# Performance work log

Hardware: AMD Instinct MI355X
Metric: run time of the kernel (lower is better)

Reference implementation:

```python
import jax, jax.numpy as jnp
import numpy as np

EPS = 1e-5
NUM_HEADS = 16

def layernorm(x, g, b):
    mu = jnp.mean(x, axis=-1, keepdims=True)
    var = jnp.mean(jnp.square(x - mu), axis=-1, keepdims=True)
    return (x - mu) * jax.lax.rsqrt(var + EPS) * g + b

def setup_inputs() -> dict:
    key = jax.random.key(0)
    ks = jax.random.split(key, 5)
    B, N, C = 2, 2048, 1024
    s_in = 1.0 / np.sqrt(C)
    return {
        "x": jax.random.normal(ks[0], (B, N, C), jnp.float32),
        "ln1_g": jnp.ones((C,), jnp.float32),
        "ln1_b": jnp.zeros((C,), jnp.float32),
        "w_qk": jax.random.normal(ks[1], (C, 2 * C), jnp.float32) * s_in,
        "w_v": jax.random.normal(ks[2], (C, C), jnp.float32) * s_in,
        "ln2_g": jnp.ones((C,), jnp.float32),
        "ln2_b": jnp.zeros((C,), jnp.float32),
        "w_proj": jax.random.normal(ks[3], (C, C), jnp.float32) * s_in,
        "b_proj": jnp.zeros((C,), jnp.float32),
    }

def reference(x, ln1_g, ln1_b, w_qk, w_v, ln2_g, ln2_b, w_proj, b_proj):
    B, N, C = x.shape
    H = NUM_HEADS
    hd = C // H
    scale = hd ** (-0.5)
    xn = layernorm(x, ln1_g, ln1_b)
    # qk: [B,N,2C] -> q,k each [B,H,N,hd]
    qk = (xn @ w_qk).reshape(B, N, 2, H, hd).transpose(2, 0, 3, 1, 4)
    q, k = qk[0], qk[1]
    v = (xn @ w_v).reshape(B, N, H, hd).transpose(0, 2, 1, 3)  # [B,H,N,hd]
    attn = jnp.einsum("bhqd,bhkd->bhqk", q, k) * scale
    attn = jax.nn.softmax(attn, axis=-1)
    out = jnp.einsum("bhqk,bhkd->bhqd", attn, v)  # [B,H,N,hd]
    out = out.transpose(0, 2, 1, 3).reshape(B, N, C)
    out = layernorm(out, ln2_g, ln2_b)
    return out @ w_proj + b_proj
```

## Files before the change

kernel.cpp:

```cpp
#include <hip/hip_runtime.h>
#include <hip/hip_bf16.h>


typedef __attribute__((ext_vector_type(8))) short short8;
typedef __attribute__((ext_vector_type(4))) short short4v;
typedef __attribute__((ext_vector_type(4))) float float4v;
typedef __attribute__((ext_vector_type(4))) unsigned uint4v;

__device__ __forceinline__ unsigned short f2bf(float f) {
    unsigned u = __builtin_bit_cast(unsigned, f);
    return (unsigned short)((u + 0x7FFFu + ((u >> 16) & 1u)) >> 16);
}
__device__ __forceinline__ unsigned packbf2(float lo, float hi) {
    return __builtin_amdgcn_perm(__builtin_bit_cast(unsigned, hi) + 0x8000u,
                                 __builtin_bit_cast(unsigned, lo) + 0x8000u,
                                 0x07060302u);
}
__device__ __forceinline__ void gll16(const unsigned short* g, unsigned short* l) {
    __builtin_amdgcn_global_load_lds(
        (const __attribute__((address_space(1))) unsigned int*)g,
        (__attribute__((address_space(3))) unsigned int*)l, 16, 0, 0);
}

__global__ __launch_bounds__(256) void prep(
    const float* __restrict__ x, const float* __restrict__ g1, const float* __restrict__ b1,
    const float* __restrict__ w_qk, const float* __restrict__ w_v,
    const float* __restrict__ w_proj, const float* __restrict__ g2,
    const float* __restrict__ b2,
    unsigned short* __restrict__ xn, unsigned short* __restrict__ wqkvT,
    unsigned short* __restrict__ wgT, float* __restrict__ u, float* __restrict__ w0) {
    __shared__ float sh[32 * 33];
    const int bid = blockIdx.x, tid = threadIdx.x;
    if (bid < 4096) {
        const float4 v = reinterpret_cast<const float4*>(x + (size_t)bid * 1024)[tid];
        float s  = v.x + v.y + v.z + v.w;
        float sq = v.x * v.x + v.y * v.y + v.z * v.z + v.w * v.w;
#pragma unroll
        for (int off = 32; off >= 1; off >>= 1) {
            s  += __shfl_xor(s, off, 64);
            sq += __shfl_xor(sq, off, 64);
        }
        const int w = tid >> 6, lane = tid & 63;
        if (lane == 0) { sh[w] = s; sh[4 + w] = sq; }
        __syncthreads();
        s  = sh[0] + sh[1] + sh[2] + sh[3];
        sq = sh[4] + sh[5] + sh[6] + sh[7];
        const float mu = s * (1.f / 1024.f);
        const float rstd = rsqrtf(sq * (1.f / 1024.f) - mu * mu + 1e-5f);
        const float4 gv = reinterpret_cast<const float4*>(g1)[tid];
        const float4 bv = reinterpret_cast<const float4*>(b1)[tid];
        ushort4 o;
        o.x = f2bf((v.x - mu) * rstd * gv.x + bv.x);
        o.y = f2bf((v.y - mu) * rstd * gv.y + bv.y);
        o.z = f2bf((v.z - mu) * rstd * gv.z + bv.z);
        o.w = f2bf((v.w - mu) * rstd * gv.w + bv.w);
        *reinterpret_cast<ushort4*>(&xn[(size_t)bid * 1024 + tid * 4]) = o;
    } else {
        const float* in; unsigned short* out; int Cc, bx, by; bool doU = false;
        if (bid < 6144)      { int t = bid - 4096; in = w_qk;   out = wqkvT;               Cc = 2048; bx = t & 63; by = t >> 6; }
        else if (bid < 7168) { int t = bid - 6144; in = w_v;    out = wqkvT + 2048 * 1024; Cc = 1024; bx = t & 31; by = t >> 5; }
        else                 { int t = bid - 7168; in = w_proj; out = wgT; doU = true;     Cc = 1024; bx = t & 31; by = t >> 5; }
        const int c0 = bx * 32, r0 = by * 32;
        const int tx = tid & 31, ty = tid >> 5;
#pragma unroll
        for (int i = 0; i < 32; i += 8)
            sh[(ty + i) * 33 + tx] = in[(size_t)(r0 + ty + i) * Cc + c0 + tx];
        __syncthreads();
        const float scale = doU ? g2[r0 + tx] : 1.f;
        const float b2v   = doU ? b2[r0 + tx] : 0.f;
#pragma unroll
        for (int i = 0; i < 32; i += 8) {
            const float raw = sh[tx * 33 + ty + i];
            const float sc  = raw * scale;
            out[(size_t)(c0 + ty + i) * 1024 + r0 + tx] = f2bf(sc);
            if (doU) {
                float pu = sc, pw = raw * b2v;
#pragma unroll
                for (int off = 1; off <= 16; off <<= 1) {
                    pu += __shfl_xor(pu, off, 64);
                    pw += __shfl_xor(pw, off, 64);
                }
                if (tx == 0) {
                    atomicAdd(&u[c0 + ty + i], pu);
                    atomicAdd(&w0[c0 + ty + i], pw);
                }
            }
        }
    }
}

__global__ __launch_bounds__(512) void gemm_qkv(const unsigned short* __restrict__ A,
                                                const unsigned short* __restrict__ Bt,
                                                unsigned short* __restrict__ qb,
                                                unsigned short* __restrict__ kb,
                                                unsigned short* __restrict__ vT) {
    __shared__ unsigned short As[2 * 256 * 64];
    __shared__ unsigned short Bs[2 * 192 * 64];
    const int tid = threadIdx.x, lane = tid & 63, w = tid >> 6;
    const int wm = (w >> 1) * 64, wn = (w & 1) * 96;
    const int quad = lane >> 4, l16 = lane & 15;
    const int ls = lane >> 3, sg = lane & 7;
    const int m0 = blockIdx.y * 256, n0 = blockIdx.x * 192;

    float4v acc[4][6];
#pragma unroll
    for (int mi = 0; mi < 4; mi++)
#pragma unroll
        for (int ni = 0; ni < 6; ni++) acc[mi][ni] = float4v{0.f, 0.f, 0.f, 0.f};

    const int g = (sg ^ ls) * 8;
#pragma unroll
    for (int i = 0; i < 4; i++)
        gll16(&A[(size_t)(m0 + w * 32 + i * 8 + ls) * 1024 + g], &As[(w * 32 + i * 8) * 64]);
#pragma unroll
    for (int i = 0; i < 3; i++)
        gll16(&Bt[(size_t)(n0 + w * 24 + i * 8 + ls) * 1024 + g], &Bs[(w * 24 + i * 8) * 64]);

#pragma unroll 1
    for (int s = 0; s < 16; s++) {
        __syncthreads();
        if (s + 1 < 16) {
            const int k0 = (s + 1) << 6;
            unsigned short* Ad = As + (((s + 1) & 1) << 14);
            unsigned short* Bd = Bs + (((s + 1) & 1) * 12288);
#pragma unroll
            for (int i = 0; i < 4; i++)
                gll16(&A[(size_t)(m0 + w * 32 + i * 8 + ls) * 1024 + k0 + g],
                      &Ad[(w * 32 + i * 8) * 64]);
#pragma unroll
            for (int i = 0; i < 3; i++)
                gll16(&Bt[(size_t)(n0 + w * 24 + i * 8 + ls) * 1024 + k0 + g],
                      &Bd[(w * 24 + i * 8) * 64]);
        }
        const unsigned short* Ac = As + ((s & 1) << 14);
        const unsigned short* Bc = Bs + ((s & 1) * 12288);
#pragma unroll
        for (int ks = 0; ks < 2; ks++) {
            short8 af[4], bfr[6];
#pragma unroll
            for (int mi = 0; mi < 4; mi++) {
                const int r = wm + mi * 16 + l16;
                af[mi] = *reinterpret_cast<const short8*>(
                    &Ac[r * 64 + ((ks * 4 + quad) ^ (r & 7)) * 8]);
            }
#pragma unroll
            for (int ni = 0; ni < 6; ni++) {
                const int r = wn + ni * 16 + l16;
                bfr[ni] = *reinterpret_cast<const short8*>(
                    &Bc[r * 64 + ((ks * 4 + quad) ^ (r & 7)) * 8]);
            }
#pragma unroll
            for (int mi = 0; mi < 4; mi++)
#pragma unroll
                for (int ni = 0; ni < 6; ni++)
                    acc[mi][ni] = __builtin_amdgcn_mfma_f32_16x16x32_bf16(
                        af[mi], bfr[ni], acc[mi][ni], 0, 0, 0);
        }
    }

    const float QSCALE = 0.125f * 1.4426950408889634f;
#pragma unroll
    for (int mi = 0; mi < 4; mi++) {
        const int row0 = m0 + wm + mi * 16 + quad * 4;
        const int b = row0 >> 11, nq = row0 & 2047;
#pragma unroll
        for (int ni = 0; ni < 6; ni++) {
            const int col = n0 + wn + ni * 16 + l16;
            if (col < 1024) {
                const int h = col >> 6, d = col & 63;
#pragma unroll
                for (int r = 0; r < 4; r++)
                    qb[(((size_t)b * 16 + h) * 2048 + nq + r) * 64 + d] =
                        f2bf(acc[mi][ni][r] * QSCALE);
            } else if (col < 2048) {
                const int c = col - 1024, h = c >> 6, d = c & 63;
#pragma unroll
                for (int r = 0; r < 4; r++)
                    kb[(((size_t)b * 16 + h) * 2048 + nq + r) * 64 + d] = f2bf(acc[mi][ni][r]);
            } else {
                const int c = col - 2048, h = c >> 6, d = c & 63;
                const short4v sv = {(short)f2bf(acc[mi][ni][0]), (short)f2bf(acc[mi][ni][1]),
                                    (short)f2bf(acc[mi][ni][2]), (short)f2bf(acc[mi][ni][3])};
                *reinterpret_cast<short4v*>(
                    &vT[(((size_t)b * 16 + h) * 64 + d) * 2048 + nq]) = sv;
            }
        }
    }
}

__global__ __launch_bounds__(256) void flash_attn(const unsigned short* __restrict__ qbuf,
                                                  const unsigned short* __restrict__ kb,
                                                  const unsigned short* __restrict__ vT,
                                                  unsigned short* __restrict__ attn,
                                                  float2* __restrict__ part) {
    __shared__ unsigned short Ks[2][64 * 64];
    __shared__ unsigned short Vs[2][64 * 64];
    const int tid = threadIdx.x, lane = tid & 63, w = tid >> 6;
    const int quad = lane >> 4, l16 = lane & 15;
    const int ls = lane >> 3, sg = lane & 7;
    const int q0 = blockIdx.x * 128, bh = blockIdx.y;
    const size_t nbase = (size_t)bh * 2048;

    int srow[2];
#pragma unroll
    for (int i = 0; i < 2; i++) {
        const int pr = w * 16 + i * 8 + ls;
        srow[i] = (pr & 32) | ((pr & 12) << 1) | ((pr & 16) >> 2) | (pr & 3);
    }
    const int sgran = (sg ^ ls) << 3;

    short8 bq[2][2];
#pragma unroll
    for (int q2 = 0; q2 < 2; q2++)
#pragma unroll
        for (int ks = 0; ks < 2; ks++)
            bq[q2][ks] = *reinterpret_cast<const short8*>(
                &qbuf[(nbase + q0 + w * 32 + q2 * 16 + l16) * 64 + ks * 32 + quad * 8]);

    float l_part[2] = {0.f, 0.f};
    float4v o_acc[2][4];
#pragma unroll
    for (int q2 = 0; q2 < 2; q2++)
#pragma unroll
        for (int db = 0; db < 4; db++) o_acc[q2][db] = float4v{0.f, 0.f, 0.f, 0.f};

#pragma unroll
    for (int i = 0; i < 2; i++) {
        gll16(&kb[(nbase + srow[i]) * 64 + sgran], &Ks[0][(w * 16 + i * 8) * 64]);
        gll16(&vT[((size_t)bh * 64 + w * 16 + i * 8 + ls) * 2048 + sgran],
              &Vs[0][(w * 16 + i * 8) * 64]);
    }

#pragma unroll 1
    for (int s = 0; s < 32; s++) {
        __syncthreads();
        if (s + 1 < 32) {
            const int ktn = (s + 1) << 6, buf = (s + 1) & 1;
#pragma unroll
            for (int i = 0; i < 2; i++) {
                gll16(&kb[(nbase + ktn + srow[i]) * 64 + sgran],
                      &Ks[buf][(w * 16 + i * 8) * 64]);
                gll16(&vT[((size_t)bh * 64 + w * 16 + i * 8 + ls) * 2048 + ktn + sgran],
                      &Vs[buf][(w * 16 + i * 8) * 64]);
            }
        }
        const unsigned short* Kc = Ks[s & 1];
        const unsigned short* Vc = Vs[s & 1];

        short8 kf[2][4];
#pragma unroll
        for (int ks = 0; ks < 2; ks++)
#pragma unroll
            for (int cb = 0; cb < 4; cb++) {
                const int r = cb * 16 + l16;
                kf[ks][cb] = *reinterpret_cast<const short8*>(
                    &Kc[r * 64 + ((ks * 4 + quad) ^ (r & 7)) * 8]);
            }
        short8 va[2][4];
#pragma unroll
        for (int k2 = 0; k2 < 2; k2++)
#pragma unroll
            for (int db = 0; db < 4; db++) {
                const int r = db * 16 + l16;
                va[k2][db] = *reinterpret_cast<const short8*>(
                    &Vc[r * 64 + ((k2 * 4 + quad) ^ (r & 7)) * 8]);
            }

#pragma unroll
        for (int q2 = 0; q2 < 2; q2++) {
            float4v s_acc[4];
#pragma unroll
            for (int cb = 0; cb < 4; cb++) s_acc[cb] = float4v{0.f, 0.f, 0.f, 0.f};
#pragma unroll
            for (int ks = 0; ks < 2; ks++)
#pragma unroll
                for (int cb = 0; cb < 4; cb++)
                    s_acc[cb] = __builtin_amdgcn_mfma_f32_16x16x32_bf16(
                        kf[ks][cb], bq[q2][ks], s_acc[cb], 0, 0, 0);

            float ls2 = 0.f;
            short8 pb[2];
#pragma unroll
            for (int k2 = 0; k2 < 2; k2++) {
                float p[8];
#pragma unroll
                for (int cc = 0; cc < 2; cc++)
#pragma unroll
                    for (int r = 0; r < 4; r++) {
                        const float pv = __builtin_amdgcn_exp2f(s_acc[k2 * 2 + cc][r]);
                        p[cc * 4 + r] = pv;
                        ls2 += pv;
                    }
                uint4v pd;
                pd.x = packbf2(p[0], p[1]); pd.y = packbf2(p[2], p[3]);
                pd.z = packbf2(p[4], p[5]); pd.w = packbf2(p[6], p[7]);
                pb[k2] = __builtin_bit_cast(short8, pd);
            }
            l_part[q2] += ls2;
#pragma unroll
            for (int k2 = 0; k2 < 2; k2++)
#pragma unroll
                for (int db = 0; db < 4; db++)
                    o_acc[q2][db] = __builtin_amdgcn_mfma_f32_16x16x32_bf16(
                        va[k2][db], pb[k2], o_acc[q2][db], 0, 0, 0);
        }
    }

    const int b = bh >> 4, h = bh & 15;
#pragma unroll
    for (int q2 = 0; q2 < 2; q2++) {
        float lr = l_part[q2];
        lr += __shfl_xor(lr, 16, 64);
        lr += __shfl_xor(lr, 32, 64);
        const float inv = 1.f / lr;
        const int grow = b * 2048 + q0 + w * 32 + q2 * 16 + l16;
        float s = 0.f, s2 = 0.f;
#pragma unroll
        for (int db = 0; db < 4; db++) {
            const float o0 = o_acc[q2][db][0] * inv, o1 = o_acc[q2][db][1] * inv;
            const float o2 = o_acc[q2][db][2] * inv, o3 = o_acc[q2][db][3] * inv;
            const ushort4 st = {f2bf(o0), f2bf(o1), f2bf(o2), f2bf(o3)};
            *reinterpret_cast<ushort4*>(
                &attn[(size_t)grow * 1024 + h * 64 + db * 16 + quad * 4]) = st;
            s  += (o0 + o1) + (o2 + o3);
            s2 += (o0 * o0 + o1 * o1) + (o2 * o2 + o3 * o3);
        }
        s  += __shfl_xor(s, 16, 64);  s  += __shfl_xor(s, 32, 64);
        s2 += __shfl_xor(s2, 16, 64); s2 += __shfl_xor(s2, 32, 64);
        if (quad == 0) part[(size_t)grow * 16 + h] = float2{s, s2};
    }
}

__global__ __launch_bounds__(256) void gemm_proj(const unsigned short* __restrict__ A,
                                                 const unsigned short* __restrict__ Bt,
                                                 const float2* __restrict__ part,
                                                 const float* __restrict__ u,
                                                 const float* __restrict__ w0,
                                                 const float* __restrict__ bias,
                                                 float* __restrict__ out) {
    __shared__ unsigned short As[2 * 128 * 64];
    __shared__ unsigned short Bs[2 * 64 * 64];
    __shared__ float2 rstat_s[128];
    const int tid = threadIdx.x, lane = tid & 63, w = tid >> 6;
    const int quad = lane >> 4, l16 = lane & 15;
    const int ls = lane >> 3, sg = lane & 7;
    const int m0 = blockIdx.y * 128, n0 = blockIdx.x * 64;
    {
        const int rloc = tid >> 1, half = tid & 1;
        const float4* p4 = reinterpret_cast<const float4*>(part);
        float s = 0.f, s2 = 0.f;
#pragma unroll
        for (int j = 0; j < 4; j++) {
            const float4 p = p4[(size_t)(m0 + rloc) * 8 + half * 4 + j];
            s += p.x + p.z; s2 += p.y + p.w;
        }
        s  += __shfl_xor(s, 1, 64);
        s2 += __shfl_xor(s2, 1, 64);
        if (!half) {
            const float mu = s * (1.f / 1024.f);
            const float rstd = rsqrtf(s2 * (1.f / 1024.f) - mu * mu + 1e-5f);
            rstat_s[rloc] = float2{rstd, mu * rstd};
        }
    }

    float4v acc[2][4];
#pragma unroll
    for (int mi = 0; mi < 2; mi++)
#pragma unroll
        for (int ni = 0; ni < 4; ni++) acc[mi][ni] = float4v{0.f, 0.f, 0.f, 0.f};

    const int g = (sg ^ ls) * 8;
#pragma unroll
    for (int i = 0; i < 4; i++)
        gll16(&A[(size_t)(m0 + w * 32 + i * 8 + ls) * 1024 + g], &As[(w * 32 + i * 8) * 64]);
#pragma unroll
    for (int i = 0; i < 2; i++)
        gll16(&Bt[(size_t)(n0 + w * 16 + i * 8 + ls) * 1024 + g], &Bs[(w * 16 + i * 8) * 64]);

#pragma unroll 1
    for (int s = 0; s < 16; s++) {
        __syncthreads();
        if (s + 1 < 16) {
            const int k0 = (s + 1) << 6;
            unsigned short* Ad = As + (((s + 1) & 1) << 13);
            unsigned short* Bd = Bs + (((s + 1) & 1) << 12);
#pragma unroll
            for (int i = 0; i < 4; i++)
                gll16(&A[(size_t)(m0 + w * 32 + i * 8 + ls) * 1024 + k0 + g],
                      &Ad[(w * 32 + i * 8) * 64]);
#pragma unroll
            for (int i = 0; i < 2; i++)
                gll16(&Bt[(size_t)(n0 + w * 16 + i * 8 + ls) * 1024 + k0 + g],
                      &Bd[(w * 16 + i * 8) * 64]);
        }
        const unsigned short* Ac = As + ((s & 1) << 13);
        const unsigned short* Bc = Bs + ((s & 1) << 12);
#pragma unroll
        for (int ks = 0; ks < 2; ks++) {
            short8 af[2], bfr[4];
#pragma unroll
            for (int mi = 0; mi < 2; mi++) {
                const int r = w * 32 + mi * 16 + l16;
                af[mi] = *reinterpret_cast<const short8*>(
                    &Ac[r * 64 + ((ks * 4 + quad) ^ (r & 7)) * 8]);
            }
#pragma unroll
            for (int ni = 0; ni < 4; ni++) {
                const int r = ni * 16 + l16;
                bfr[ni] = *reinterpret_cast<const short8*>(
                    &Bc[r * 64 + ((ks * 4 + quad) ^ (r & 7)) * 8]);
            }
#pragma unroll
            for (int mi = 0; mi < 2; mi++)
#pragma unroll
                for (int ni = 0; ni < 4; ni++)
                    acc[mi][ni] = __builtin_amdgcn_mfma_f32_16x16x32_bf16(
                        af[mi], bfr[ni], acc[mi][ni], 0, 0, 0);
        }
    }

#pragma unroll
    for (int mi = 0; mi < 2; mi++) {
        const int rl0 = w * 32 + mi * 16 + quad * 4;
        float2 rs[4];
#pragma unroll
        for (int r = 0; r < 4; r++) rs[r] = rstat_s[rl0 + r];
#pragma unroll
        for (int ni = 0; ni < 4; ni++) {
            const int col = n0 + ni * 16 + l16;
            const float uu = u[col], ww = w0[col] + bias[col];
#pragma unroll
            for (int r = 0; r < 4; r++)
                out[(size_t)(m0 + rl0 + r) * 1024 + col] =
                    fmaf(rs[r].x, acc[mi][ni][r], ww - rs[r].y * uu);
        }
    }
}

extern "C" void kernel_launch(void* const* d_in, const int* in_sizes, int n_in,
                              void* d_out, int out_size, void* d_ws, size_t ws_size,
                              hipStream_t stream) {
    const float* x      = (const float*)d_in[0];
    const float* ln1_g  = (const float*)d_in[1];
    const float* ln1_b  = (const float*)d_in[2];
    const float* w_qk   = (const float*)d_in[3];
    const float* w_v    = (const float*)d_in[4];
    const float* ln2_g  = (const float*)d_in[5];
    const float* ln2_b  = (const float*)d_in[6];
    const float* w_proj = (const float*)d_in[7];
    const float* b_proj = (const float*)d_in[8];
    float* out = (float*)d_out;

    char* ws = (char*)d_ws;
    unsigned short* xn      = (unsigned short*)(ws + 0);
    unsigned short* wqkvT   = (unsigned short*)(ws + 8388608);
    unsigned short* wgT     = (unsigned short*)(ws + 14680064);
    unsigned short* qbuf    = (unsigned short*)(ws + 16777216);
    unsigned short* kbuf    = (unsigned short*)(ws + 25165824);
    unsigned short* vTbuf   = (unsigned short*)(ws + 33554432);
    unsigned short* attn    = (unsigned short*)(ws + 41943040);
    float2*         part    = (float2*)(ws + 50331648);
    float*          u       = (float*)(ws + 50888704);
    float*          w0      = (float*)(ws + 50892800);

    hipMemsetAsync(ws + 50888704, 0, 8192, stream);
    prep<<<8192, 256, 0, stream>>>(x, ln1_g, ln1_b, w_qk, w_v, w_proj, ln2_g, ln2_b,
                                   xn, wqkvT, wgT, u, w0);
    gemm_qkv<<<dim3(16, 16), 512, 0, stream>>>(xn, wqkvT, qbuf, kbuf, vTbuf);
    flash_attn<<<dim3(16, 32), 256, 0, stream>>>(qbuf, kbuf, vTbuf, attn, part);
    gemm_proj<<<dim3(16, 32), 256, 0, stream>>>(attn, wgT, part, u, w0, b_proj, out);
}
```

Measured before the change: 192.7 us.

## Split flash attention key tiles across two wave groups with LDS reduction

Doubles the attention block to 512 threads, so each pair of waves shares a 32-row query tile and splits every 64-key tile into two 32-key halves. The partial outputs and row sums are then combined through shared memory at the end. It also switches the bf16 packing to the hardware v_cvt_pk_bf16_f32 instruction and raises MFMA priority with s_setprio. The aim is more waves in flight to hide latency, at the cost of an extra LDS reduction, a barrier, and half the MFMA work per wave.

Measured after the change: 191.9 us. No clear change (-0.4%).

```diff
diff --git a/kernel.cpp b/kernel.cpp
--- a/kernel.cpp
+++ b/kernel.cpp
@@ -15,6 +15,11 @@
     return __builtin_amdgcn_perm(__builtin_bit_cast(unsigned, hi) + 0x8000u,
                                  __builtin_bit_cast(unsigned, lo) + 0x8000u,
                                  0x07060302u);
+}
+__device__ __forceinline__ unsigned cvtpk(float lo, float hi) {
+    unsigned r;
+    asm("v_cvt_pk_bf16_f32 %0, %1, %2" : "=v"(r) : "v"(lo), "v"(hi));
+    return r;
 }
 __device__ __forceinline__ void gll16(const unsigned short* g, unsigned short* l) {
     __builtin_amdgcn_global_load_lds(
@@ -188,25 +193,22 @@
     }
 }
 
-__global__ __launch_bounds__(256) void flash_attn(const unsigned short* __restrict__ qbuf,
-                                                  const unsigned short* __restrict__ kb,
-                                                  const unsigned short* __restrict__ vT,
-                                                  unsigned short* __restrict__ attn,
-                                                  float2* __restrict__ part) {
-    __shared__ unsigned short Ks[2][64 * 64];
-    __shared__ unsigned short Vs[2][64 * 64];
+__global__ __launch_bounds__(512, 4) void flash_attn(const unsigned short* __restrict__ qbuf,
+                                                     const unsigned short* __restrict__ kb,
+                                                     const unsigned short* __restrict__ vT,
+                                                     unsigned short* __restrict__ attn,
+                                                     float2* __restrict__ part) {
+    __shared__ __align__(16) unsigned short KV[4][64 * 64];
+    __shared__ float lsh[4][2][64];
     const int tid = threadIdx.x, lane = tid & 63, w = tid >> 6;
+    const int wq = w & 3, kh = w >> 2;
     const int quad = lane >> 4, l16 = lane & 15;
     const int ls = lane >> 3, sg = lane & 7;
     const int q0 = blockIdx.x * 128, bh = blockIdx.y;
     const size_t nbase = (size_t)bh * 2048;
 
-    int srow[2];
-#pragma unroll
-    for (int i = 0; i < 2; i++) {
-        const int pr = w * 16 + i * 8 + ls;
-        srow[i] = (pr & 32) | ((pr & 12) << 1) | ((pr & 16) >> 2) | (pr & 3);
-    }
+    const int pr = w * 8 + ls;
+    const int srow = (pr & 32) | ((pr & 12) << 1) | ((pr & 16) >> 2) | (pr & 3);
     const int sgran = (sg ^ ls) << 3;
 
     short8 bq[2][2];
@@ -215,7 +217,7 @@
 #pragma unroll
         for (int ks = 0; ks < 2; ks++)
             bq[q2][ks] = *reinterpret_cast<const short8*>(
-                &qbuf[(nbase + q0 + w * 32 + q2 * 16 + l16) * 64 + ks * 32 + quad * 8]);
+                &qbuf[(nbase + q0 + wq * 32 + q2 * 16 + l16) * 64 + ks * 32 + quad * 8]);
 
     float l_part[2] = {0.f, 0.f};
     float4v o_acc[2][4];
@@ -224,110 +226,119 @@
 #pragma unroll
         for (int db = 0; db < 4; db++) o_acc[q2][db] = float4v{0.f, 0.f, 0.f, 0.f};
 
-#pragma unroll
-    for (int i = 0; i < 2; i++) {
-        gll16(&kb[(nbase + srow[i]) * 64 + sgran], &Ks[0][(w * 16 + i * 8) * 64]);
-        gll16(&vT[((size_t)bh * 64 + w * 16 + i * 8 + ls) * 2048 + sgran],
-              &Vs[0][(w * 16 + i * 8) * 64]);
-    }
+    gll16(&kb[(nbase + srow) * 64 + sgran], &KV[0][w * 8 * 64]);
+    gll16(&vT[((size_t)bh * 64 + w * 8 + ls) * 2048 + sgran], &KV[2][w * 8 * 64]);
 
 #pragma unroll 1
     for (int s = 0; s < 32; s++) {
         __syncthreads();
         if (s + 1 < 32) {
             const int ktn = (s + 1) << 6, buf = (s + 1) & 1;
-#pragma unroll
-            for (int i = 0; i < 2; i++) {
-                gll16(&kb[(nbase + ktn + srow[i]) * 64 + sgran],
-                      &Ks[buf][(w * 16 + i * 8) * 64]);
-                gll16(&vT[((size_t)bh * 64 + w * 16 + i * 8 + ls) * 2048 + ktn + sgran],
-                      &Vs[buf][(w * 16 + i * 8) * 64]);
-            }
-        }
-        const unsigned short* Kc = Ks[s & 1];
-        const unsigned short* Vc = Vs[s & 1];
-
-        short8 kf[2][4];
+            gll16(&kb[(nbase + ktn + srow) * 64 + sgran], &KV[buf][w * 8 * 64]);
+            gll16(&vT[((size_t)bh * 64 + w * 8 + ls) * 2048 + ktn + sgran],
+                  &KV[2 + buf][w * 8 * 64]);
+        }
+        const unsigned short* Kc = KV[s & 1];
+        const unsigned short* Vc = KV[2 + (s & 1)];
+
+        short8 kf[2][2];
 #pragma unroll
         for (int ks = 0; ks < 2; ks++)
 #pragma unroll
-            for (int cb = 0; cb < 4; cb++) {
-                const int r = cb * 16 + l16;
-                kf[ks][cb] = *reinterpret_cast<const short8*>(
+            for (int cc = 0; cc < 2; cc++) {
+                const int r = kh * 32 + cc * 16 + l16;
+                kf[ks][cc] = *reinterpret_cast<const short8*>(
                     &Kc[r * 64 + ((ks * 4 + quad) ^ (r & 7)) * 8]);
             }
-        short8 va[2][4];
-#pragma unroll
-        for (int k2 = 0; k2 < 2; k2++)
+        short8 va[4];
+#pragma unroll
+        for (int db = 0; db < 4; db++) {
+            const int r = db * 16 + l16;
+            va[db] = *reinterpret_cast<const short8*>(
+                &Vc[r * 64 + ((kh * 4 + quad) ^ (r & 7)) * 8]);
+        }
+
+#pragma unroll
+        for (int q2 = 0; q2 < 2; q2++) {
+            float4v s_acc[2];
+#pragma unroll
+            for (int cc = 0; cc < 2; cc++) s_acc[cc] = float4v{0.f, 0.f, 0.f, 0.f};
+            __builtin_amdgcn_s_setprio(1);
+#pragma unroll
+            for (int ks = 0; ks < 2; ks++)
+#pragma unroll
+                for (int cc = 0; cc < 2; cc++)
+                    s_acc[cc] = __builtin_amdgcn_mfma_f32_16x16x32_bf16(
+                        kf[ks][cc], bq[q2][ks], s_acc[cc], 0, 0, 0);
+            __builtin_amdgcn_s_setprio(0);
+
+            float ls2 = 0.f;
+            float p[8];
+#pragma unroll
+            for (int cc = 0; cc < 2; cc++)
+#pragma unroll
+                for (int r = 0; r < 4; r++) {
+                    const float pv = __builtin_amdgcn_exp2f(s_acc[cc][r]);
+                    p[cc * 4 + r] = pv;
+                    ls2 += pv;
+                }
+            uint4v pd;
+            pd.x = cvtpk(p[0], p[1]); pd.y = cvtpk(p[2], p[3]);
+            pd.z = cvtpk(p[4], p[5]); pd.w = cvtpk(p[6], p[7]);
+            const short8 pb = __builtin_bit_cast(short8, pd);
+            l_part[q2] += ls2;
+            __builtin_amdgcn_s_setprio(1);
+#pragma unroll
+            for (int db = 0; db < 4; db++)
+                o_acc[q2][db] = __builtin_amdgcn_mfma_f32_16x16x32_bf16(
+                    va[db], pb, o_acc[q2][db], 0, 0, 0);
+            __builtin_amdgcn_s_setprio(0);
+        }
+    }
+
+    __syncthreads();
+    float* osh = reinterpret_cast<float*>(KV);
+    const int swz = (l16 & 7) << 2;
+    if (kh == 1) {
+#pragma unroll
+        for (int q2 = 0; q2 < 2; q2++)
 #pragma unroll
             for (int db = 0; db < 4; db++) {
-                const int r = db * 16 + l16;
-                va[k2][db] = *reinterpret_cast<const short8*>(
-                    &Vc[r * 64 + ((k2 * 4 + quad) ^ (r & 7)) * 8]);
-            }
-
+                const int base = (wq * 32 + q2 * 16 + l16) * 64 + db * 16 + quad * 4;
+                *reinterpret_cast<float4v*>(&osh[base ^ swz]) = o_acc[q2][db];
+            }
+        lsh[wq][0][lane] = l_part[0];
+        lsh[wq][1][lane] = l_part[1];
+    }
+    __syncthreads();
+    if (kh == 0) {
+        const int b = bh >> 4, h = bh & 15;
 #pragma unroll
         for (int q2 = 0; q2 < 2; q2++) {
-            float4v s_acc[4];
-#pragma unroll
-            for (int cb = 0; cb < 4; cb++) s_acc[cb] = float4v{0.f, 0.f, 0.f, 0.f};
-#pragma unroll
-            for (int ks = 0; ks < 2; ks++)
-#pragma unroll
-                for (int cb = 0; cb < 4; cb++)
-                    s_acc[cb] = __builtin_amdgcn_mfma_f32_16x16x32_bf16(
-                        kf[ks][cb], bq[q2][ks], s_acc[cb], 0, 0, 0);
-
-            float ls2 = 0.f;
-            short8 pb[2];
-#pragma unroll
-            for (int k2 = 0; k2 < 2; k2++) {
-                float p[8];
-#pragma unroll
-                for (int cc = 0; cc < 2; cc++)
-#pragma unroll
-                    for (int r = 0; r < 4; r++) {
-                        const float pv = __builtin_amdgcn_exp2f(s_acc[k2 * 2 + cc][r]);
-                        p[cc * 4 + r] = pv;
-                        ls2 += pv;
-                    }
-                uint4v pd;
-                pd.x = packbf2(p[0], p[1]); pd.y = packbf2(p[2], p[3]);
-                pd.z = packbf2(p[4], p[5]); pd.w = packbf2(p[6], p[7]);
-                pb[k2] = __builtin_bit_cast(short8, pd);
-            }
-            l_part[q2] += ls2;
-#pragma unroll
-            for (int k2 = 0; k2 < 2; k2++)
-#pragma unroll
-                for (int db = 0; db < 4; db++)
-                    o_acc[q2][db] = __builtin_amdgcn_mfma_f32_16x16x32_bf16(
-                        va[k2][db], pb[k2], o_acc[q2][db], 0, 0, 0);
-        }
-    }
-
-    const int b = bh >> 4, h = bh & 15;
-#pragma unroll
-    for (int q2 = 0; q2 < 2; q2++) {
-        float lr = l_part[q2];
-        lr += __shfl_xor(lr, 16, 64);
-        lr += __shfl_xor(lr, 32, 64);
-        const float inv = 1.f / lr;
-        const int grow = b * 2048 + q0 + w * 32 + q2 * 16 + l16;
-        float s = 0.f, s2 = 0.f;
-#pragma unroll
-        for (int db = 0; db < 4; db++) {
-            const float o0 = o_acc[q2][db][0] * inv, o1 = o_acc[q2][db][1] * inv;
-            const float o2 = o_acc[q2][db][2] * inv, o3 = o_acc[q2][db][3] * inv;
-            const ushort4 st = {f2bf(o0), f2bf(o1), f2bf(o2), f2bf(o3)};
-            *reinterpret_cast<ushort4*>(
-                &attn[(size_t)grow * 1024 + h * 64 + db * 16 + quad * 4]) = st;
-            s  += (o0 + o1) + (o2 + o3);
-            s2 += (o0 * o0 + o1 * o1) + (o2 * o2 + o3 * o3);
-        }
-        s  += __shfl_xor(s, 16, 64);  s  += __shfl_xor(s, 32, 64);
-        s2 += __shfl_xor(s2, 16, 64); s2 += __shfl_xor(s2, 32, 64);
-        if (quad == 0) part[(size_t)grow * 16 + h] = float2{s, s2};
+            float lr = l_part[q2] + lsh[wq][q2][lane];
+            lr += __shfl_xor(lr, 16, 64);
+            lr += __shfl_xor(lr, 32, 64);
+            const float inv = 1.f / lr;
+            const int grow = b * 2048 + q0 + wq * 32 + q2 * 16 + l16;
+            float sum = 0.f, s2 = 0.f;
+#pragma unroll
+            for (int db = 0; db < 4; db++) {
+                const int base = (wq * 32 + q2 * 16 + l16) * 64 + db * 16 + quad * 4;
+                const float4v oh = *reinterpret_cast<const float4v*>(&osh[base ^ swz]);
+                const float o0 = (o_acc[q2][db][0] + oh[0]) * inv;
+                const float o1 = (o_acc[q2][db][1] + oh[1]) * inv;
+                const float o2 = (o_acc[q2][db][2] + oh[2]) * inv;
+                const float o3 = (o_acc[q2][db][3] + oh[3]) * inv;
+                const ushort4 st = {f2bf(o0), f2bf(o1), f2bf(o2), f2bf(o3)};
+                *reinterpret_cast<ushort4*>(
+                    &attn[(size_t)grow * 1024 + h * 64 + db * 16 + quad * 4]) = st;
+                sum += (o0 + o1) + (o2 + o3);
+                s2  += (o0 * o0 + o1 * o1) + (o2 * o2 + o3 * o3);
+            }
+            sum += __shfl_xor(sum, 16, 64); sum += __shfl_xor(sum, 32, 64);
+            s2  += __shfl_xor(s2, 16, 64);  s2  += __shfl_xor(s2, 32, 64);
+            if (quad == 0) part[(size_t)grow * 16 + h] = float2{sum, s2};
+        }
     }
 }
 
@@ -467,6 +478,6 @@
     prep<<<8192, 256, 0, stream>>>(x, ln1_g, ln1_b, w_qk, w_v, w_proj, ln2_g, ln2_b,
                                    xn, wqkvT, wgT, u, w0);
     gemm_qkv<<<dim3(16, 16), 512, 0, stream>>>(xn, wqkvT, qbuf, kbuf, vTbuf);
-    flash_attn<<<dim3(16, 32), 256, 0, stream>>>(qbuf, kbuf, vTbuf, attn, part);
+    flash_attn<<<dim3(16, 32), 512, 0, stream>>>(qbuf, kbuf, vTbuf, attn, part);
     gemm_proj<<<dim3(16, 32), 256, 0, stream>>>(attn, wgT, part, u, w0, b_proj, out);
 }
```
